# Performance work log

Hardware: AMD Instinct MI355X
Metric: run time of the kernel (lower is better)

Reference implementation:

```python
import jax, jax.numpy as jnp
import numpy as np

BATCH = 2
SEQ = 2048
D_MODEL = 512
D_STATE = 16
D_CONV = 4
D_INNER = 2 * D_MODEL  # expand=2


def setup_inputs() -> dict:
    key = jax.random.key(0)
    ks = jax.random.split(key, 7)
    s = 0.02
    x = jax.random.normal(ks[0], (BATCH, SEQ, D_MODEL), jnp.float32)
    W_in = jax.random.normal(ks[1], (2 * D_INNER, D_MODEL), jnp.float32) * s
    conv_w = jax.random.normal(ks[2], (D_INNER, 1, D_CONV), jnp.float32) * s  # depthwise kernel
    conv_b = jnp.zeros((D_INNER,), jnp.float32)
    W_x = jax.random.normal(ks[3], (2 * D_STATE, D_INNER), jnp.float32) * s
    W_dt = jax.random.normal(ks[4], (D_INNER, D_INNER), jnp.float32) * s
    b_dt = jnp.zeros((D_INNER,), jnp.float32)
    # A_log init: log of [1..d_state] broadcast over d_inner rows
    A_log = jnp.log(jnp.broadcast_to(jnp.arange(1, D_STATE + 1, dtype=jnp.float32), (D_INNER, D_STATE)))
    D_param = jnp.ones((D_INNER,), jnp.float32)
    W_out = jax.random.normal(ks[5], (D_MODEL, D_INNER), jnp.float32) * s
    return dict(x=x, W_in=W_in, conv_w=conv_w, conv_b=conv_b, W_x=W_x,
                W_dt=W_dt, b_dt=b_dt, A_log=A_log, D_param=D_param, W_out=W_out)


def reference(x, W_in, conv_w, conv_b, W_x, W_dt, b_dt, A_log, D_param, W_out):
    # in_proj, split into x-branch and gate z
    xz = x @ W_in.T                             # [B, L, 2*di]
    xi, z = jnp.split(xz, 2, axis=-1)
    # depthwise causal conv1d (torch pads both sides then slices [:seq_len] == left-pad only)
    h = jnp.transpose(xi, (0, 2, 1))            # [B, di, L]
    h = jax.lax.conv_general_dilated(
        h, conv_w, window_strides=(1,), padding=[(D_CONV - 1, 0)],
        dimension_numbers=('NCH', 'OIH', 'NCH'), feature_group_count=D_INNER)
    h = h + conv_b[None, :, None]
    h = jax.nn.silu(jnp.transpose(h, (0, 2, 1)))  # [B, L, di]

    A = -jnp.exp(A_log)                         # [di, ds]
    x_dbl = h @ W_x.T                           # [B, L, 2*ds]
    _delta_unused, Bmat = jnp.split(x_dbl, 2, axis=-1)  # B (also used as C): [B, L, ds]
    delta = jax.nn.softplus(h @ W_dt.T + b_dt)  # [B, L, di] (overwrites x_proj delta, as in source)

    def step(state, inp):
        d_t, B_t, h_t = inp                     # [B,di], [B,ds], [B,di]
        dA = jnp.exp(d_t[:, :, None] * A)       # [B, di, ds]
        state = dA * state + d_t[:, :, None] * B_t[:, None, :] * h_t[:, :, None]
        y_t = jnp.einsum('bds,bs->bd', state, B_t)  # C == B
        return state, y_t

    init = jnp.zeros((x.shape[0], D_INNER, D_STATE), x.dtype)
    _, ys = jax.lax.scan(step, init,
                         (jnp.swapaxes(delta, 0, 1), jnp.swapaxes(Bmat, 0, 1), jnp.swapaxes(h, 0, 1)))
    y = jnp.swapaxes(ys, 0, 1)                  # [B, L, di]
    y = (y + D_param * h) * jax.nn.silu(z)
    return y @ W_out.T                          # [B, L, d_model]
```

## Files before the change

### kernel.cpp

```cpp
#include <hip/hip_runtime.h>
#include <cstddef>
#include <cstdint>

#define NB 2
#define L_SEQ 2048
#define DM 512
#define DS 16
#define DI 1024
#define NC 64
#define CL (L_SEQ/NC)

typedef __attribute__((ext_vector_type(4))) float f32x4;
typedef __attribute__((ext_vector_type(8))) short bf16x8;

__device__ __forceinline__ float softplus_f(float x) {
  return (x > 20.f) ? x : log1pf(expf(x));
}
__device__ __forceinline__ float silu_f(float x) {
  return x / (1.f + expf(-x));
}
__device__ __forceinline__ ushort f2bf(float f) {
  uint32_t u = __float_as_uint(f);
  return (ushort)((u + 0x7fffu + ((u >> 16) & 1u)) >> 16);
}
__device__ __forceinline__ float bf2f(ushort h) {
  return __uint_as_float(((uint32_t)h) << 16);
}

__device__ __forceinline__ void gload16(const void* g, ushort* lds_wave_base) {
  __builtin_amdgcn_global_load_lds(
      (const __attribute__((address_space(1))) void*)g,
      (__attribute__((address_space(3))) void*)lds_wave_base, 16, 0, 0);
}

__device__ __forceinline__ void split4(const float4 v, ushort4* hi, ushort4* lo) {
  ushort h0 = f2bf(v.x), h1 = f2bf(v.y), h2 = f2bf(v.z), h3 = f2bf(v.w);
  *hi = make_ushort4(h0, h1, h2, h3);
  *lo = make_ushort4(f2bf(v.x - bf2f(h0)), f2bf(v.y - bf2f(h1)),
                     f2bf(v.z - bf2f(h2)), f2bf(v.w - bf2f(h3)));
}

__global__ __launch_bounds__(256) void split_all(
    const float* __restrict__ x,    ushort* __restrict__ xh,  ushort* __restrict__ xl,
    const float* __restrict__ win,  ushort* __restrict__ wih, ushort* __restrict__ wil,
    const float* __restrict__ wdt,  ushort* __restrict__ wdh, ushort* __restrict__ wdl,
    const float* __restrict__ wx,   ushort* __restrict__ wxh, ushort* __restrict__ wxl,
    const float* __restrict__ wout, ushort* __restrict__ woh, ushort* __restrict__ wol) {
  int bi = blockIdx.x;
  const float* in; ushort* hi; ushort* lo; int i;
  if (bi < 2048)      { in = x;    hi = xh;  lo = xl;  i = bi * 256 + threadIdx.x; }
  else if (bi < 3072) { in = win;  hi = wih; lo = wil; i = (bi - 2048) * 256 + threadIdx.x; }
  else if (bi < 4096) { in = wdt;  hi = wdh; lo = wdl; i = (bi - 3072) * 256 + threadIdx.x; }
  else if (bi < 4112) { in = wx;   hi = wxh; lo = wxl; i = (bi - 4096) * 256 + threadIdx.x; }
  else                { in = wout; hi = woh; lo = wol; i = (bi - 4112) * 256 + threadIdx.x; }
  float4 v = ((const float4*)in)[i];
  ushort4 h4, l4;
  split4(v, &h4, &l4);
  ((ushort4*)hi)[i] = h4;
  ((ushort4*)lo)[i] = l4;
}

#define MFMA(a, b, c) __builtin_amdgcn_mfma_f32_16x16x32_bf16((a), (b), (c), 0, 0, 0)

template <int ACT>
__global__ __launch_bounds__(512, 4) void gemm_mfma8(
    const ushort* __restrict__ Ahi, const ushort* __restrict__ Alo, int lda,
    const ushort* __restrict__ Bhi, const ushort* __restrict__ Blo, int ldb,
    const float* __restrict__ bias, float* __restrict__ C, int ldc,
    float* __restrict__ Bmout, int K) {
  constexpr int BM = 128, BN = 64;
  constexpr int AT = BM * 32;
  constexpr int BT = BN * 32;
  constexpr int BUF = 2 * AT + 2 * BT;
  constexpr int MR = 2, NR = 2;
  __shared__ __align__(16) ushort lds[3 * BUF];

  const int tid = threadIdx.x;
  const int lane = tid & 63;
  const int wave = tid >> 6;
  const int wr = wave >> 1;
  const int wc = wave & 1;

  const int nx = gridDim.x;
  const int nwg = nx * gridDim.y;
  int bid = blockIdx.y * nx + blockIdx.x;
  bid = (bid & 7) * (nwg >> 3) + (bid >> 3);
  const int m0 = (bid / nx) * BM;
  const int n0 = (bid % nx) * BN;

  const int ra = tid >> 2;
  const int kga = (tid & 3) ^ ((ra >> 1) & 3);
  const size_t aoff = (size_t)(m0 + ra) * lda + kga * 8;
  const int tq = tid & 255;
  const int rb = tq >> 2;
  const int kgb = (tq & 3) ^ ((rb >> 1) & 3);
  const size_t boff = (size_t)(n0 + rb) * ldb + kgb * 8;
  const ushort* Bsel = (wave < 4) ? Bhi : Blo;
  const int blds = 2 * AT + ((wave < 4) ? wave * 512 : BT + (wave - 4) * 512);

  const int fr = lane & 15, fq = lane >> 4;
  const int kswz = fq ^ ((fr >> 1) & 3);
  int aoffs[MR], boffs[NR];
#pragma unroll
  for (int m = 0; m < MR; m++) aoffs[m] = (wr * 32 + m * 16 + fr) * 32 + kswz * 8;
#pragma unroll
  for (int n = 0; n < NR; n++) boffs[n] = (wc * 32 + n * 16 + fr) * 32 + kswz * 8;

  f32x4 acc[MR][NR];
#pragma unroll
  for (int m = 0; m < MR; m++)
#pragma unroll
    for (int n = 0; n < NR; n++) acc[m][n] = (f32x4){0.f, 0.f, 0.f, 0.f};

  const int nsteps = K >> 5;

#define STAGE(base, kk)                                     \
  {                                                         \
    ushort* bp = (base);                                    \
    gload16(Ahi + aoff + (kk), bp + wave * 512);            \
    gload16(Alo + aoff + (kk), bp + AT + wave * 512);       \
    gload16(Bsel + boff + (kk), bp + blds);                 \
  }

#define COMPUTE(base)                                                          \
  {                                                                            \
    const ushort* cp = (base);                                                 \
    bf16x8 ah[MR], al[MR], bh[NR], bl[NR];                                     \
    _Pragma("unroll")                                                          \
    for (int m = 0; m < MR; m++) ah[m] = *(const bf16x8*)(cp + aoffs[m]);      \
    _Pragma("unroll")                                                          \
    for (int m = 0; m < MR; m++) al[m] = *(const bf16x8*)(cp + AT + aoffs[m]); \
    _Pragma("unroll")                                                          \
    for (int n = 0; n < NR; n++) bh[n] = *(const bf16x8*)(cp + 2 * AT + boffs[n]); \
    _Pragma("unroll")                                                          \
    for (int n = 0; n < NR; n++) bl[n] = *(const bf16x8*)(cp + 2 * AT + BT + boffs[n]); \
    _Pragma("unroll")                                                          \
    for (int m = 0; m < MR; m++)                                               \
      _Pragma("unroll")                                                        \
      for (int n = 0; n < NR; n++)                                             \
        acc[m][n] = MFMA(ah[m], bh[n], acc[m][n]);                             \
    _Pragma("unroll")                                                          \
    for (int m = 0; m < MR; m++)                                               \
      _Pragma("unroll")                                                        \
      for (int n = 0; n < NR; n++)                                             \
        acc[m][n] = MFMA(al[m], bh[n], acc[m][n]);                             \
    _Pragma("unroll")                                                          \
    for (int m = 0; m < MR; m++)                                               \
      _Pragma("unroll")                                                        \
      for (int n = 0; n < NR; n++)                                             \
        acc[m][n] = MFMA(ah[m], bl[n], acc[m][n]);                             \
  }

  STAGE(lds, 0);
  STAGE(lds + BUF, 32);
  int ocur = 0, onext = BUF, ofar = 2 * BUF;
  for (int t = 0; t < nsteps; ++t) {
    if (t == nsteps - 1) asm volatile("s_waitcnt vmcnt(0)" ::: "memory");
    else                 asm volatile("s_waitcnt vmcnt(3)" ::: "memory");
    __builtin_amdgcn_s_barrier();
    if (t + 2 < nsteps) STAGE(lds + ofar, (t + 2) << 5);
    COMPUTE(lds + ocur);
    int tmp = ocur; ocur = onext; onext = ofar; ofar = tmp;
  }
#undef STAGE
#undef COMPUTE

#pragma unroll
  for (int m = 0; m < MR; m++) {
    const int row = m0 + wr * 32 + m * 16 + fq * 4;
#pragma unroll
    for (int n = 0; n < NR; n++) {
      const int col = n0 + wc * 32 + n * 16 + fr;
      if (ACT == 1) {
        if (col < DI) {
          const float bcol = bias[col];
#pragma unroll
          for (int j = 0; j < 4; j++)
            C[(size_t)(row + j) * ldc + col] = softplus_f(acc[m][n][j] + bcol);
        } else if (col < DI + DS) {
#pragma unroll
          for (int j = 0; j < 4; j++)
            Bmout[(size_t)(row + j) * DS + (col - DI)] = acc[m][n][j];
        }
      } else {
#pragma unroll
        for (int j = 0; j < 4; j++)
          C[(size_t)(row + j) * ldc + col] = acc[m][n][j];
      }
    }
  }
}

__global__ __launch_bounds__(256, 3) void gemm_mfma4(
    const ushort* __restrict__ Ahi, const ushort* __restrict__ Alo, int lda,
    const ushort* __restrict__ Bhi, const ushort* __restrict__ Blo, int ldb,
    float* __restrict__ C, int ldc, int K) {
  constexpr int BM = 64, BN = 64;
  constexpr int AT = BM * 32;
  constexpr int BT = BN * 32;
  constexpr int BUF = 2 * AT + 2 * BT;
  constexpr int MR = 2, NR = 2;
  __shared__ __align__(16) ushort lds[3 * BUF];

  const int tid = threadIdx.x;
  const int lane = tid & 63;
  const int wave = tid >> 6;
  const int wr = wave >> 1, wc = wave & 1;

  const int nx = gridDim.x;
  const int nwg = nx * gridDim.y;
  int bid = blockIdx.y * nx + blockIdx.x;
  bid = (bid & 7) * (nwg >> 3) + (bid >> 3);
  const int m0 = (bid / nx) * BM;
  const int n0 = (bid % nx) * BN;

  const int r0 = tid >> 2;
  const int kg = (tid & 3) ^ ((r0 >> 1) & 3);
  const size_t aoff = (size_t)(m0 + r0) * lda + kg * 8;
  const size_t boff = (size_t)(n0 + r0) * ldb + kg * 8;

  const int fr = lane & 15, fq = lane >> 4;
  const int kswz = fq ^ ((fr >> 1) & 3);
  int aoffs[MR], boffs[NR];
#pragma unroll
  for (int m = 0; m < MR; m++) aoffs[m] = (wr * 32 + m * 16 + fr) * 32 + kswz * 8;
#pragma unroll
  for (int n = 0; n < NR; n++) boffs[n] = (wc * 32 + n * 16 + fr) * 32 + kswz * 8;

  f32x4 acc[MR][NR];
#pragma unroll
  for (int m = 0; m < MR; m++)
#pragma unroll
    for (int n = 0; n < NR; n++) acc[m][n] = (f32x4){0.f, 0.f, 0.f, 0.f};

  const int nsteps = K >> 5;

#define STAGE4(base, kk)                                          \
  {                                                               \
    ushort* bp = (base);                                          \
    gload16(Ahi + aoff + (kk), bp + wave * 512);                  \
    gload16(Alo + aoff + (kk), bp + AT + wave * 512);             \
    gload16(Bhi + boff + (kk), bp + 2 * AT + wave * 512);         \
    gload16(Blo + boff + (kk), bp + 2 * AT + BT + wave * 512);    \
  }

#define COMPUTE4(base)                                                         \
  {                                                                            \
    const ushort* cp = (base);                                                 \
    bf16x8 ah[MR], al[MR], bh[NR], bl[NR];                                     \
    _Pragma("unroll")                                                          \
    for (int m = 0; m < MR; m++) ah[m] = *(const bf16x8*)(cp + aoffs[m]);      \
    _Pragma("unroll")                                                          \
    for (int m = 0; m < MR; m++) al[m] = *(const bf16x8*)(cp + AT + aoffs[m]); \
    _Pragma("unroll")                                                          \
    for (int n = 0; n < NR; n++) bh[n] = *(const bf16x8*)(cp + 2 * AT + boffs[n]); \
    _Pragma("unroll")                                                          \
    for (int n = 0; n < NR; n++) bl[n] = *(const bf16x8*)(cp + 2 * AT + BT + boffs[n]); \
    _Pragma("unroll")                                                          \
    for (int m = 0; m < MR; m++)                                               \
      _Pragma("unroll")                                                        \
      for (int n = 0; n < NR; n++)                                             \
        acc[m][n] = MFMA(ah[m], bh[n], acc[m][n]);                             \
    _Pragma("unroll")                                                          \
    for (int m = 0; m < MR; m++)                                               \
      _Pragma("unroll")                                                        \
      for (int n = 0; n < NR; n++)                                             \
        acc[m][n] = MFMA(al[m], bh[n], acc[m][n]);                             \
    _Pragma("unroll")                                                          \
    for (int m = 0; m < MR; m++)                                               \
      _Pragma("unroll")                                                        \
      for (int n = 0; n < NR; n++)                                             \
        acc[m][n] = MFMA(ah[m], bl[n], acc[m][n]);                             \
  }

  STAGE4(lds, 0);
  STAGE4(lds + BUF, 32);
  int ocur = 0, onext = BUF, ofar = 2 * BUF;
  for (int t = 0; t < nsteps; ++t) {
    if (t == nsteps - 1) asm volatile("s_waitcnt vmcnt(0)" ::: "memory");
    else                 asm volatile("s_waitcnt vmcnt(4)" ::: "memory");
    __builtin_amdgcn_s_barrier();
    if (t + 2 < nsteps) STAGE4(lds + ofar, (t + 2) << 5);
    COMPUTE4(lds + ocur);
    int tmp = ocur; ocur = onext; onext = ofar; ofar = tmp;
  }
#undef STAGE4
#undef COMPUTE4

#pragma unroll
  for (int m = 0; m < MR; m++) {
    const int row = m0 + wr * 32 + m * 16 + fq * 4;
#pragma unroll
    for (int n = 0; n < NR; n++) {
      const int col = n0 + wc * 32 + n * 16 + fr;
#pragma unroll
      for (int j = 0; j < 4; j++)
        C[(size_t)(row + j) * ldc + col] = acc[m][n][j];
    }
  }
}

__global__ __launch_bounds__(256) void conv_silu_kernel(
    const float* __restrict__ xz, const float* __restrict__ conv_w,
    const float* __restrict__ conv_b, float* __restrict__ h,
    ushort* __restrict__ h_hi, ushort* __restrict__ h_lo) {
  const int idx = blockIdx.x * 256 + threadIdx.x;
  const int c = idx & (DI - 1);
  const int r = idx >> 10;
  const int l = r & (L_SEQ - 1);
  const float w0 = conv_w[c * 4 + 0];
  const float w1 = conv_w[c * 4 + 1];
  const float w2 = conv_w[c * 4 + 2];
  const float w3 = conv_w[c * 4 + 3];
  const float* xp = xz + (size_t)r * (2 * DI) + c;
  float acc = conv_b[c];
  if (l >= 3) acc += xp[-3 * 2 * DI] * w0;
  if (l >= 2) acc += xp[-2 * 2 * DI] * w1;
  if (l >= 1) acc += xp[-1 * 2 * DI] * w2;
  acc += xp[0] * w3;
  const float hv = silu_f(acc);
  h[idx] = hv;
  const ushort hh = f2bf(hv);
  h_hi[idx] = hh;
  h_lo[idx] = f2bf(hv - bf2f(hh));
}

__global__ __launch_bounds__(256) void scan_phase1(
    const float* __restrict__ delta, const float* __restrict__ h,
    const float* __restrict__ Bm, const float* __restrict__ A_log,
    float* __restrict__ aprod, float* __restrict__ blocal) {
  __shared__ float sB[CL * DS];
  const int tid = threadIdx.x;
  const int bid = blockIdx.x;
  const int cblk = bid & 3;
  const int chunk = (bid >> 2) & (NC - 1);
  const int b = bid >> 8;
  const int c = cblk * 256 + tid;
  const size_t row0 = (size_t)b * L_SEQ + chunk * CL;
  ((float2*)sB)[tid] = ((const float2*)(Bm + row0 * DS))[tid];
  __syncthreads();

  float Acs[DS], state[DS];
#pragma unroll
  for (int s = 0; s < DS; s += 4) {
    float4 al = *(const float4*)(A_log + (size_t)c * DS + s);
    Acs[s + 0] = -__expf(al.x);
    Acs[s + 1] = -__expf(al.y);
    Acs[s + 2] = -__expf(al.z);
    Acs[s + 3] = -__expf(al.w);
    state[s + 0] = 0.f; state[s + 1] = 0.f; state[s + 2] = 0.f; state[s + 3] = 0.f;
  }
  const float* dp = delta + row0 * DI + c;
  const float* hp = h + row0 * DI + c;
  float sdt = 0.f;
  for (int t = 0; t < CL; ++t) {
    const float dt = dp[(size_t)t * DI];
    const float ht = hp[(size_t)t * DI];
    const float dth = dt * ht;
    sdt += dt;
#pragma unroll
    for (int s = 0; s < DS; ++s)
      state[s] = __expf(dt * Acs[s]) * state[s] + dth * sB[t * DS + s];
  }
  const size_t o = (((size_t)b * NC + chunk) * DI + c) * DS;
#pragma unroll
  for (int s = 0; s < DS; s += 4) {
    *(float4*)(aprod + o + s) = make_float4(
        __expf(Acs[s] * sdt), __expf(Acs[s + 1] * sdt),
        __expf(Acs[s + 2] * sdt), __expf(Acs[s + 3] * sdt));
    *(float4*)(blocal + o + s) = make_float4(state[s], state[s + 1], state[s + 2], state[s + 3]);
  }
}

__global__ __launch_bounds__(256) void scan_phase2(
    float* __restrict__ aprod, const float* __restrict__ blocal) {
  const int idx = blockIdx.x * 256 + threadIdx.x;
  const int b = idx >> 14;
  const int cs = idx & 16383;
  float st = 0.f;
  for (int ch = 0; ch < NC; ++ch) {
    const size_t o = (size_t)(b * NC + ch) * (DI * DS) + cs;
    const float a = aprod[o];
    const float bl = blocal[o];
    aprod[o] = st;
    st = a * st + bl;
  }
}

__global__ __launch_bounds__(256) void scan_phase3(
    const float* __restrict__ delta, const float* __restrict__ h,
    const float* __restrict__ Bm, const float* __restrict__ A_log,
    const float* __restrict__ sinit, float* __restrict__ xz,
    const float* __restrict__ Dp) {
  __shared__ float sB[CL * DS];
  const int tid = threadIdx.x;
  const int bid = blockIdx.x;
  const int cblk = bid & 3;
  const int chunk = (bid >> 2) & (NC - 1);
  const int b = bid >> 8;
  const int c = cblk * 256 + tid;
  const size_t row0 = (size_t)b * L_SEQ + chunk * CL;
  ((float2*)sB)[tid] = ((const float2*)(Bm + row0 * DS))[tid];
  __syncthreads();

  float Acs[DS], state[DS];
  const size_t o = (((size_t)b * NC + chunk) * DI + c) * DS;
#pragma unroll
  for (int s = 0; s < DS; s += 4) {
    float4 al = *(const float4*)(A_log + (size_t)c * DS + s);
    Acs[s + 0] = -__expf(al.x);
    Acs[s + 1] = -__expf(al.y);
    Acs[s + 2] = -__expf(al.z);
    Acs[s + 3] = -__expf(al.w);
    float4 sv = *(const float4*)(sinit + o + s);
    state[s + 0] = sv.x; state[s + 1] = sv.y; state[s + 2] = sv.z; state[s + 3] = sv.w;
  }
  const float* dp = delta + row0 * DI + c;
  const float* hp = h + row0 * DI + c;
  const float* zp = xz + row0 * (2 * DI) + DI + c;
  ushort* yrow = (ushort*)(xz + row0 * (2 * DI)) + c;
  const float Dc = Dp[c];
  for (int t = 0; t < CL; ++t) {
    const float dt = dp[(size_t)t * DI];
    const float ht = hp[(size_t)t * DI];
    const float z = zp[(size_t)t * (2 * DI)];
    const float dth = dt * ht;
    float yv = 0.f;
#pragma unroll
    for (int s = 0; s < DS; ++s) {
      const float bt = sB[t * DS + s];
      state[s] = __expf(dt * Acs[s]) * state[s] + dth * bt;
      yv += state[s] * bt;
    }
    const float g = (yv + Dc * ht) * silu_f(z);
    const ushort gh = f2bf(g);
    yrow[(size_t)t * 4096] = gh;
    yrow[(size_t)t * 4096 + 1024] = f2bf(g - bf2f(gh));
  }
}

extern "C" void kernel_launch(void* const* d_in, const int* in_sizes, int n_in,
                              void* d_out, int out_size, void* d_ws, size_t ws_size,
                              hipStream_t stream) {
  const float* x      = (const float*)d_in[0];
  const float* W_in   = (const float*)d_in[1];
  const float* conv_w = (const float*)d_in[2];
  const float* conv_b = (const float*)d_in[3];
  const float* W_x    = (const float*)d_in[4];
  const float* W_dt   = (const float*)d_in[5];
  const float* b_dt   = (const float*)d_in[6];
  const float* A_log  = (const float*)d_in[7];
  const float* D_par  = (const float*)d_in[8];
  const float* W_out  = (const float*)d_in[9];
  float* out = (float*)d_out;

  float* xz     = (float*)d_ws;
  float* h      = xz + (size_t)(8u << 20);
  float* delta  = h + (size_t)(4u << 20);
  float* Bm     = delta + (size_t)(4u << 20);
  ushort* W2hi  = (ushort*)(Bm + (size_t)(64u << 10));
  ushort* W2lo  = W2hi + (size_t)1088 * 1024;
  ushort* Wout_hi = W2lo + (size_t)1088 * 1024;
  ushort* Wout_lo = Wout_hi + (size_t)(512u << 10);
  float* xreg   = (float*)(Wout_lo + (size_t)(512u << 10));
  ushort* x_hi  = (ushort*)xreg;
  ushort* x_lo  = x_hi + (size_t)(2u << 20);
  ushort* Win_hi = x_lo + (size_t)(2u << 20);
  ushort* Win_lo = Win_hi + (size_t)(1u << 20);
  ushort* h_hi  = (ushort*)xreg;
  ushort* h_lo  = h_hi + (size_t)(4u << 20);
  float* aprod  = xreg;
  float* blocal = aprod + (size_t)(2u << 20);
  ushort* y_hi  = (ushort*)xz;
  ushort* y_lo  = y_hi + 1024;

  const int rows = NB * L_SEQ;

  split_all<<<4624, 256, 0, stream>>>(
      x, x_hi, x_lo, W_in, Win_hi, Win_lo, W_dt, W2hi, W2lo,
      W_x + DS * DI, W2hi + (size_t)DI * DI, W2lo + (size_t)DI * DI,
      W_out, Wout_hi, Wout_lo);

  gemm_mfma8<0><<<dim3(32, 32), 512, 0, stream>>>(
      x_hi, x_lo, DM, Win_hi, Win_lo, DM, nullptr, xz, 2 * DI, nullptr, DM);
  conv_silu_kernel<<<(rows * DI) / 256, 256, 0, stream>>>(xz, conv_w, conv_b, h, h_hi, h_lo);
  gemm_mfma8<1><<<dim3(17, 32), 512, 0, stream>>>(
      h_hi, h_lo, DI, W2hi, W2lo, DI, b_dt, delta, DI, Bm, DI);
  scan_phase1<<<NB * NC * (DI / 256), 256, 0, stream>>>(delta, h, Bm, A_log, aprod, blocal);
  scan_phase2<<<(NB * DI * DS) / 256, 256, 0, stream>>>(aprod, blocal);
  scan_phase3<<<NB * NC * (DI / 256), 256, 0, stream>>>(delta, h, Bm, A_log, aprod, xz, D_par);
  gemm_mfma4<<<dim3(8, 64), 256, 0, stream>>>(
      y_hi, y_lo, 4096, Wout_hi, Wout_lo, DI, out, DM, DI);
}
```

Baseline: 200.7 us.

## Fuse three scan phases into one cooperative kernel with grid syncs

Replaces the three chunked-scan launches with a single cooperative kernel of 256 blocks of 512 threads. Each thread keeps its chunk's delta and h values in registers across two grid-wide syncs, so phase 3 does not re-read them from global memory, and two kernel launches go away. In exchange it uses a large per-thread register footprint (dt/ht arrays of 32 each). Each block covers 512 channels instead of 256, so there are far fewer blocks than before, and the cooperative launch falls back to the old path on failure.

Result: slower. 409.2 us (+103.9%).

```diff
diff --git a/kernel.cpp b/kernel.cpp
--- a/kernel.cpp
+++ b/kernel.cpp
@@ -1,6 +1,9 @@
 #include <hip/hip_runtime.h>
+#include <hip/hip_cooperative_groups.h>
 #include <cstddef>
 #include <cstdint>
+
+namespace cg = cooperative_groups;
 
 #define NB 2
 #define L_SEQ 2048
@@ -439,6 +442,98 @@
   }
 }
 
+__global__ __launch_bounds__(512, 2) void scan_fused(
+    const float* __restrict__ delta, const float* __restrict__ h,
+    const float* __restrict__ Bm, const float* __restrict__ A_log,
+    float* __restrict__ aprod, float* __restrict__ blocal,
+    float* __restrict__ xz, const float* __restrict__ Dp) {
+  __shared__ float sB[CL * DS];
+  const int tid = threadIdx.x;
+  const int bid = blockIdx.x;
+  const int cgrp = bid & 1;
+  const int chunk = (bid >> 1) & (NC - 1);
+  const int b = bid >> 7;
+  const int c = cgrp * 512 + tid;
+  const size_t row0 = (size_t)b * L_SEQ + chunk * CL;
+  sB[tid] = Bm[row0 * DS + tid];
+  __syncthreads();
+
+  float Acs[DS], state[DS], dt[CL], ht[CL];
+#pragma unroll
+  for (int s = 0; s < DS; s += 4) {
+    float4 al = *(const float4*)(A_log + (size_t)c * DS + s);
+    Acs[s + 0] = -__expf(al.x);
+    Acs[s + 1] = -__expf(al.y);
+    Acs[s + 2] = -__expf(al.z);
+    Acs[s + 3] = -__expf(al.w);
+    state[s + 0] = 0.f; state[s + 1] = 0.f; state[s + 2] = 0.f; state[s + 3] = 0.f;
+  }
+  const float* dp = delta + row0 * DI + c;
+  const float* hp = h + row0 * DI + c;
+  float sdt = 0.f;
+#pragma unroll
+  for (int t = 0; t < CL; ++t) {
+    dt[t] = dp[(size_t)t * DI];
+    ht[t] = hp[(size_t)t * DI];
+    const float dth = dt[t] * ht[t];
+    sdt += dt[t];
+#pragma unroll
+    for (int s = 0; s < DS; ++s)
+      state[s] = __expf(dt[t] * Acs[s]) * state[s] + dth * sB[t * DS + s];
+  }
+  const size_t o = (((size_t)b * NC + chunk) * DI + c) * DS;
+#pragma unroll
+  for (int s = 0; s < DS; s += 4) {
+    *(float4*)(aprod + o + s) = make_float4(
+        __expf(Acs[s] * sdt), __expf(Acs[s + 1] * sdt),
+        __expf(Acs[s + 2] * sdt), __expf(Acs[s + 3] * sdt));
+    *(float4*)(blocal + o + s) = make_float4(state[s], state[s + 1], state[s + 2], state[s + 3]);
+  }
+
+  cg::this_grid().sync();
+
+  const int gidx = bid * 512 + tid;
+  if (gidx < NB * DI * DS) {
+    const int b2 = gidx >> 14;
+    const int cs = gidx & 16383;
+    float st = 0.f;
+    for (int ch = 0; ch < NC; ++ch) {
+      const size_t oo = (size_t)(b2 * NC + ch) * (DI * DS) + cs;
+      const float a = aprod[oo];
+      const float bl = blocal[oo];
+      aprod[oo] = st;
+      st = a * st + bl;
+    }
+  }
+
+  cg::this_grid().sync();
+
+#pragma unroll
+  for (int s = 0; s < DS; s += 4) {
+    float4 sv = *(const float4*)(aprod + o + s);
+    state[s + 0] = sv.x; state[s + 1] = sv.y; state[s + 2] = sv.z; state[s + 3] = sv.w;
+  }
+  const float* zp = xz + row0 * (2 * DI) + DI + c;
+  ushort* yrow = (ushort*)(xz + row0 * (2 * DI)) + c;
+  const float Dc = Dp[c];
+#pragma unroll
+  for (int t = 0; t < CL; ++t) {
+    const float z = zp[(size_t)t * (2 * DI)];
+    const float dth = dt[t] * ht[t];
+    float yv = 0.f;
+#pragma unroll
+    for (int s = 0; s < DS; ++s) {
+      const float bt = sB[t * DS + s];
+      state[s] = __expf(dt[t] * Acs[s]) * state[s] + dth * bt;
+      yv += state[s] * bt;
+    }
+    const float g = (yv + Dc * ht[t]) * silu_f(z);
+    const ushort gh = f2bf(g);
+    yrow[(size_t)t * 4096] = gh;
+    yrow[(size_t)t * 4096 + 1024] = f2bf(g - bf2f(gh));
+  }
+}
+
 extern "C" void kernel_launch(void* const* d_in, const int* in_sizes, int n_in,
                               void* d_out, int out_size, void* d_ws, size_t ws_size,
                               hipStream_t stream) {
@@ -486,9 +581,18 @@
   conv_silu_kernel<<<(rows * DI) / 256, 256, 0, stream>>>(xz, conv_w, conv_b, h, h_hi, h_lo);
   gemm_mfma8<1><<<dim3(17, 32), 512, 0, stream>>>(
       h_hi, h_lo, DI, W2hi, W2lo, DI, b_dt, delta, DI, Bm, DI);
-  scan_phase1<<<NB * NC * (DI / 256), 256, 0, stream>>>(delta, h, Bm, A_log, aprod, blocal);
-  scan_phase2<<<(NB * DI * DS) / 256, 256, 0, stream>>>(aprod, blocal);
-  scan_phase3<<<NB * NC * (DI / 256), 256, 0, stream>>>(delta, h, Bm, A_log, aprod, xz, D_par);
+  {
+    const float* delta_c = delta; const float* h_c = h; const float* Bm_c = Bm;
+    void* args[] = {(void*)&delta_c, (void*)&h_c, (void*)&Bm_c, (void*)&A_log,
+                    (void*)&aprod, (void*)&blocal, (void*)&xz, (void*)&D_par};
+    hipError_t e = hipLaunchCooperativeKernel((void*)scan_fused, dim3(256),
+                                              dim3(512), args, 0, stream);
+    if (e != hipSuccess) {
+      scan_phase1<<<NB * NC * (DI / 256), 256, 0, stream>>>(delta, h, Bm, A_log, aprod, blocal);
+      scan_phase2<<<(NB * DI * DS) / 256, 256, 0, stream>>>(aprod, blocal);
+      scan_phase3<<<NB * NC * (DI / 256), 256, 0, stream>>>(delta, h, Bm, A_log, aprod, xz, D_par);
+    }
+  }
   gemm_mfma4<<<dim3(8, 64), 256, 0, stream>>>(
       y_hi, y_lo, 4096, Wout_hi, Wout_lo, DI, out, DM, DI);
 }
```
